# Optimization experiments

Measured on AMD Instinct MI355X. Metric: run time of the kernel, lower is better.

The kernel has to match this reference:

```python
import math
import jax, jax.numpy as jnp
import numpy as np

B, S, H, V = 8, 1024, 768, 8192  # V = max_verses

def setup_inputs() -> dict:
    key = jax.random.key(0)
    k1, k2, k3, k4 = jax.random.split(key, 4)
    hidden_states = jax.random.normal(k1, (B, S, H), dtype=jnp.float32)
    verse_ids = jax.random.randint(k2, (B, S), 0, V + 1)  # 0 = no verse
    cross_ref_matrix = jax.random.normal(k3, (V + 1, V + 1), dtype=jnp.float32) * 0.02
    out_w = jax.random.normal(k4, (H, H), dtype=jnp.float32) * (1.0 / math.sqrt(H))
    out_b = jnp.zeros((H,), dtype=jnp.float32)
    ln_w = jnp.ones((H,), dtype=jnp.float32)
    ln_b = jnp.zeros((H,), dtype=jnp.float32)
    return {"hidden_states": hidden_states, "verse_ids": verse_ids,
            "cross_ref_matrix": cross_ref_matrix, "out_w": out_w, "out_b": out_b,
            "ln_w": ln_w, "ln_b": ln_b}

def _layer_norm(x, w, b, eps=1e-5):
    mu = jnp.mean(x, axis=-1, keepdims=True)
    var = jnp.var(x, axis=-1, keepdims=True)
    return (x - mu) * jax.lax.rsqrt(var + eps) * w + b

def reference(hidden_states, verse_ids, cross_ref_matrix, out_w, out_b, ln_w, ln_b):
    h = hidden_states.shape[-1]
    has = verse_ids > 0                              # [B,S]
    # position_scores[b,i,j] = M[verse_ids[b,i], verse_ids[b,j]] where both have a verse, else 0
    scores = cross_ref_matrix[verse_ids[:, :, None], verse_ids[:, None, :]]  # [B,S,S] gather
    mask = has[:, :, None] & has[:, None, :]
    scores = jnp.where(mask, scores, 0.0) * (1.0 / math.sqrt(h))
    # NOTE: faithful to original — masked entries are 0 (NOT -inf) inside the softmax
    attn = jax.nn.softmax(scores, axis=-1)           # [B,S,S]; dropout is identity at eval
    ctx = jnp.einsum('bij,bjd->bid', attn, hidden_states)  # bmm
    proj = jnp.einsum('bid,od->bio', ctx, out_w) + out_b   # torch Linear: x @ W^T + b
    return _layer_norm(hidden_states + proj, ln_w, ln_b)
```

## Files before the change

### kernel.cpp

```cpp
#include <hip/hip_runtime.h>
#include <hip/hip_bf16.h>


namespace {
constexpr int kS = 1024;
constexpr int kH = 768;
constexpr int kV = 8193;
}

typedef __attribute__((ext_vector_type(8))) short short8;
typedef __attribute__((ext_vector_type(4))) float f32x4;

__device__ __forceinline__ unsigned short f2bf(float f) {
  union { float f; unsigned u; } v; v.f = f;
  unsigned r = v.u + 0x7FFFu + ((v.u >> 16) & 1u);
  return (unsigned short)(r >> 16);
}

__device__ __forceinline__ void async_lds16(const void* gsrc, void* ldst) {
  __builtin_amdgcn_global_load_lds(
      (const __attribute__((address_space(1))) unsigned int*)gsrc,
      (__attribute__((address_space(3))) unsigned int*)ldst, 16, 0, 0);
}

__global__ __launch_bounds__(256) void convert_w(const float* __restrict__ w,
                                                 unsigned short* __restrict__ wb) {
  int i = blockIdx.x * 256 + threadIdx.x;
  float4 v = reinterpret_cast<const float4*>(w)[i];
  ushort4 o;
  o.x = f2bf(v.x); o.y = f2bf(v.y); o.z = f2bf(v.z); o.w = f2bf(v.w);
  reinterpret_cast<ushort4*>(wb)[i] = o;
}

__global__ __launch_bounds__(256) void gather_softmax(const int* __restrict__ ids,
                                                      const float* __restrict__ Mx,
                                                      unsigned short* __restrict__ P) {
  const int i = blockIdx.x, b = blockIdx.y;
  const int t = threadIdx.x;
  const int sid = ids[b * kS + i];
  const float scale = 0.036084391824351615f;
  const float* Mrow = Mx + (long)sid * kV;
  float e[4];
  float lsum = 0.f;
#pragma unroll
  for (int q = 0; q < 4; ++q) {
    int j = t + q * 256;
    int cj = ids[b * kS + j];
    float v = 1.0f;
    if (sid > 0 && cj > 0) v = __expf(Mrow[cj] * scale);
    e[q] = v; lsum += v;
  }
#pragma unroll
  for (int o = 32; o; o >>= 1) lsum += __shfl_down(lsum, o);
  __shared__ float red[4];
  if ((t & 63) == 0) red[t >> 6] = lsum;
  __syncthreads();
  float denom = red[0] + red[1] + red[2] + red[3];
  float inv = 1.0f / denom;
  unsigned short* Pr = P + ((long)b * kS + i) * kS;
#pragma unroll
  for (int q = 0; q < 4; ++q) Pr[t + q * 256] = f2bf(e[q] * inv);
}

__global__ __launch_bounds__(256) void transpose_h(const float* __restrict__ hidden,
                                                   unsigned short* __restrict__ hT) {
  __shared__ float tile[32][33];
  const int b = blockIdx.z;
  const int h0 = blockIdx.x * 32;
  const int s0 = blockIdx.y * 32;
  const int t = threadIdx.x;
  const int c = t & 31, r0 = t >> 5;
  const float* src = hidden + (long)b * kS * kH;
#pragma unroll
  for (int q = 0; q < 4; ++q) {
    int r = r0 + q * 8;
    tile[r][c] = src[(long)(s0 + r) * kH + h0 + c];
  }
  __syncthreads();
  unsigned short* dst = hT + (long)b * kH * kS;
#pragma unroll
  for (int q = 0; q < 4; ++q) {
    int hh = r0 + q * 8;
    dst[(long)(h0 + hh) * kS + s0 + c] = f2bf(tile[c][hh]);
  }
}

__global__ __launch_bounds__(256) void gemm_nt(
    const unsigned short* __restrict__ A, long aBatchStride,
    const unsigned short* __restrict__ Bt, long bBatchStride,
    unsigned short* __restrict__ Cb, float* __restrict__ Cf,
    long cBatchStride, int N, int K, int outIsBf16) {
  __shared__ __align__(1024) unsigned short lds[6144];
  const int b = blockIdx.z;
  const int bn = blockIdx.x, bm = blockIdx.y;
  const unsigned short* Ab = A + (long)b * aBatchStride;
  const unsigned short* Bb = Bt + (long)b * bBatchStride;
  const int t = threadIdx.x;
  const int w = t >> 6, lane = t & 63;
  const int wr = w >> 1, wc = w & 1;
  const int lrow = lane & 15, kq = lane >> 4;

  const int r = t >> 2, ch = t & 3;
  const unsigned short* gA = Ab + (long)(bm * 64 + r) * K + ch * 8;
  const unsigned short* gB0 = Bb + (long)(bn * 128 + r) * K + ch * 8;
  const unsigned short* gB1 = gB0 + (long)64 * K;
  unsigned short* ldsA_dst = &lds[w * 512];
  unsigned short* ldsB0_dst = &lds[2048 + w * 512];
  unsigned short* ldsB1_dst = &lds[4096 + w * 512];

  f32x4 acc[2][4];
#pragma unroll
  for (int mi = 0; mi < 2; ++mi)
#pragma unroll
    for (int ni = 0; ni < 4; ++ni) acc[mi][ni] = (f32x4){0.f, 0.f, 0.f, 0.f};

  const int nk = K >> 5;
  for (int kt = 0; kt < nk; ++kt) {
    async_lds16(gA, ldsA_dst);
    async_lds16(gB0, ldsB0_dst);
    async_lds16(gB1, ldsB1_dst);
    gA += 32; gB0 += 32; gB1 += 32;
    __syncthreads();
    short8 af[2], bfr[4];
#pragma unroll
    for (int mi = 0; mi < 2; ++mi)
      af[mi] = *reinterpret_cast<const short8*>(&lds[(wr * 32 + mi * 16 + lrow) * 32 + kq * 8]);
#pragma unroll
    for (int ni = 0; ni < 4; ++ni)
      bfr[ni] = *reinterpret_cast<const short8*>(&lds[2048 + (wc * 64 + ni * 16 + lrow) * 32 + kq * 8]);
#pragma unroll
    for (int mi = 0; mi < 2; ++mi)
#pragma unroll
      for (int ni = 0; ni < 4; ++ni)
        acc[mi][ni] = __builtin_amdgcn_mfma_f32_16x16x32_bf16(af[mi], bfr[ni], acc[mi][ni], 0, 0, 0);
    __syncthreads();
  }

  const int row0 = bm * 64 + wr * 32;
  const int col0 = bn * 128 + wc * 64;
#pragma unroll
  for (int mi = 0; mi < 2; ++mi)
#pragma unroll
    for (int ni = 0; ni < 4; ++ni)
#pragma unroll
      for (int rg = 0; rg < 4; ++rg) {
        int row = row0 + mi * 16 + kq * 4 + rg;
        int col = col0 + ni * 16 + lrow;
        long off = (long)b * cBatchStride + (long)row * N + col;
        float v = acc[mi][ni][rg];
        if (outIsBf16) Cb[off] = f2bf(v);
        else Cf[off] = v;
      }
}

__global__ __launch_bounds__(256) void residual_ln(
    const float* __restrict__ hidden, const float* __restrict__ proj,
    const float* __restrict__ ob, const float* __restrict__ lw,
    const float* __restrict__ lb, float* __restrict__ out) {
  const long row = blockIdx.x;
  const float* h = hidden + row * kH;
  const float* p = proj + row * kH;
  const int t = threadIdx.x;
  float x[3];
  float s = 0.f, sq = 0.f;
#pragma unroll
  for (int q = 0; q < 3; ++q) {
    int c = t + q * 256;
    float v = h[c] + p[c] + ob[c];
    x[q] = v; s += v; sq += v * v;
  }
#pragma unroll
  for (int o = 32; o; o >>= 1) { s += __shfl_down(s, o); sq += __shfl_down(sq, o); }
  __shared__ float rs[4], rq[4];
  if ((t & 63) == 0) { rs[t >> 6] = s; rq[t >> 6] = sq; }
  __syncthreads();
  float ts = rs[0] + rs[1] + rs[2] + rs[3];
  float tq = rq[0] + rq[1] + rq[2] + rq[3];
  const float invH = 1.0f / 768.0f;
  float mu = ts * invH;
  float var = tq * invH - mu * mu;
  float rstd = rsqrtf(var + 1e-5f);
#pragma unroll
  for (int q = 0; q < 3; ++q) {
    int c = t + q * 256;
    out[row * kH + c] = (x[q] - mu) * rstd * lw[c] + lb[c];
  }
}

extern "C" void kernel_launch(void* const* d_in, const int* in_sizes, int n_in,
                              void* d_out, int out_size, void* d_ws, size_t ws_size,
                              hipStream_t stream) {
  const float* hidden = (const float*)d_in[0];
  const int* ids      = (const int*)d_in[1];
  const float* Mx     = (const float*)d_in[2];
  const float* out_w  = (const float*)d_in[3];
  const float* out_b  = (const float*)d_in[4];
  const float* ln_w   = (const float*)d_in[5];
  const float* ln_b   = (const float*)d_in[6];
  float* out = (float*)d_out;

  char* ws = (char*)d_ws;
  const long szP = 16777216L, szHT = 12582912L, szCTX = 12582912L;
  unsigned short* P   = (unsigned short*)ws;
  unsigned short* hT  = (unsigned short*)(ws + szP);
  unsigned short* ctx = (unsigned short*)(ws + szP + szHT);
  unsigned short* Wb  = (unsigned short*)(ws + szP + szHT + szCTX);
  float* proj = (float*)ws;

  convert_w<<<576, 256, 0, stream>>>(out_w, Wb);
  gather_softmax<<<dim3(1024, 8), 256, 0, stream>>>(ids, Mx, P);
  transpose_h<<<dim3(24, 32, 8), 256, 0, stream>>>(hidden, hT);
  gemm_nt<<<dim3(6, 16, 8), 256, 0, stream>>>(
      P, (long)kS * kS, hT, (long)kH * kS, ctx, nullptr, (long)kS * kH, kH, kS, 1);
  gemm_nt<<<dim3(6, 16, 8), 256, 0, stream>>>(
      ctx, (long)kS * kH, Wb, 0L, nullptr, proj, (long)kS * kH, kH, kH, 0);
  residual_ln<<<8192, 256, 0, stream>>>(hidden, proj, out_b, ln_w, ln_b, out);
}
```

Baseline: 469.2 us.

## Stage cross-ref row in LDS, enlarge GEMM tiles, vectorize softmax store and LayerNorm

The gather-softmax kernel now copies the whole 8193-float cross-reference row into LDS with coalesced loads, loads the verse ids as int4, and stores probabilities as ushort4. This replaces scattered global gathers. The GEMM block tile grows from 64x128 to 128x128, with a 4x4 MFMA fragment per wave and the output type made a template parameter. This raises data reuse per LDS load but halves the block count. The residual LayerNorm uses 192 threads with float4 loads and stores. Staging the row costs 32KB of LDS per block and copies the full row even though only 1024 entries are read, which may lower occupancy and add memory traffic.

```diff
diff --git a/kernel.cpp b/kernel.cpp
--- a/kernel.cpp
+++ b/kernel.cpp
@@ -35,31 +35,39 @@
 __global__ __launch_bounds__(256) void gather_softmax(const int* __restrict__ ids,
                                                       const float* __restrict__ Mx,
                                                       unsigned short* __restrict__ P) {
+  __shared__ float row[kV];
+  __shared__ float red[4];
   const int i = blockIdx.x, b = blockIdx.y;
   const int t = threadIdx.x;
   const int sid = ids[b * kS + i];
+  if (sid > 0) {
+    const float* src = Mx + (long)sid * kV;
+#pragma unroll
+    for (int q = 0; q < 32; ++q) row[t + q * 256] = src[t + q * 256];
+    if (t == 0) row[8192] = src[8192];
+  }
+  __syncthreads();
+  const int4 cj4 = reinterpret_cast<const int4*>(ids + b * kS)[t];
+  const int cj[4] = {cj4.x, cj4.y, cj4.z, cj4.w};
   const float scale = 0.036084391824351615f;
-  const float* Mrow = Mx + (long)sid * kV;
   float e[4];
   float lsum = 0.f;
 #pragma unroll
   for (int q = 0; q < 4; ++q) {
-    int j = t + q * 256;
-    int cj = ids[b * kS + j];
     float v = 1.0f;
-    if (sid > 0 && cj > 0) v = __expf(Mrow[cj] * scale);
+    if (sid > 0 && cj[q] > 0) v = __expf(row[cj[q]] * scale);
     e[q] = v; lsum += v;
   }
 #pragma unroll
   for (int o = 32; o; o >>= 1) lsum += __shfl_down(lsum, o);
-  __shared__ float red[4];
   if ((t & 63) == 0) red[t >> 6] = lsum;
   __syncthreads();
-  float denom = red[0] + red[1] + red[2] + red[3];
-  float inv = 1.0f / denom;
-  unsigned short* Pr = P + ((long)b * kS + i) * kS;
-#pragma unroll
-  for (int q = 0; q < 4; ++q) Pr[t + q * 256] = f2bf(e[q] * inv);
+  const float denom = red[0] + red[1] + red[2] + red[3];
+  const float inv = 1.0f / denom;
+  ushort4 o;
+  o.x = f2bf(e[0] * inv); o.y = f2bf(e[1] * inv);
+  o.z = f2bf(e[2] * inv); o.w = f2bf(e[3] * inv);
+  reinterpret_cast<ushort4*>(P + ((long)b * kS + i) * kS)[t] = o;
 }
 
 __global__ __launch_bounds__(256) void transpose_h(const float* __restrict__ hidden,
@@ -85,106 +93,100 @@
   }
 }
 
+template <int OUT_BF16>
 __global__ __launch_bounds__(256) void gemm_nt(
-    const unsigned short* __restrict__ A, long aBatchStride,
-    const unsigned short* __restrict__ Bt, long bBatchStride,
-    unsigned short* __restrict__ Cb, float* __restrict__ Cf,
-    long cBatchStride, int N, int K, int outIsBf16) {
-  __shared__ __align__(1024) unsigned short lds[6144];
-  const int b = blockIdx.z;
-  const int bn = blockIdx.x, bm = blockIdx.y;
-  const unsigned short* Ab = A + (long)b * aBatchStride;
-  const unsigned short* Bb = Bt + (long)b * bBatchStride;
-  const int t = threadIdx.x;
-  const int w = t >> 6, lane = t & 63;
-  const int wr = w >> 1, wc = w & 1;
+    const unsigned short* __restrict__ A, long aStride,
+    const unsigned short* __restrict__ Bt, long bStride,
+    void* __restrict__ C, long cStride, int N, int K) {
+  __shared__ __align__(1024) unsigned short lds[8192];
+  const int b = blockIdx.z, bn = blockIdx.x, bm = blockIdx.y;
+  const unsigned short* Ab = A + (long)b * aStride + (long)(bm * 128) * K;
+  const unsigned short* Bb = Bt + (long)b * bStride + (long)(bn * 128) * K;
+  const int t = threadIdx.x;
+  const int lane = t & 63;
+  const int wr = (t >> 7) & 1, wc = (t >> 6) & 1;
   const int lrow = lane & 15, kq = lane >> 4;
-
-  const int r = t >> 2, ch = t & 3;
-  const unsigned short* gA = Ab + (long)(bm * 64 + r) * K + ch * 8;
-  const unsigned short* gB0 = Bb + (long)(bn * 128 + r) * K + ch * 8;
-  const unsigned short* gB1 = gB0 + (long)64 * K;
-  unsigned short* ldsA_dst = &lds[w * 512];
-  unsigned short* ldsB0_dst = &lds[2048 + w * 512];
-  unsigned short* ldsB1_dst = &lds[4096 + w * 512];
-
-  f32x4 acc[2][4];
-#pragma unroll
-  for (int mi = 0; mi < 2; ++mi)
+  const int srow = t >> 2, scol = (t & 3) * 8;
+  char* ldsb = (char*)lds;
+
+  f32x4 acc[4][4];
+#pragma unroll
+  for (int mi = 0; mi < 4; ++mi)
 #pragma unroll
     for (int ni = 0; ni < 4; ++ni) acc[mi][ni] = (f32x4){0.f, 0.f, 0.f, 0.f};
 
-  const int nk = K >> 5;
-  for (int kt = 0; kt < nk; ++kt) {
-    async_lds16(gA, ldsA_dst);
-    async_lds16(gB0, ldsB0_dst);
-    async_lds16(gB1, ldsB1_dst);
-    gA += 32; gB0 += 32; gB1 += 32;
+  for (int kt = 0; kt < K; kt += 32) {
+#pragma unroll
+    for (int q = 0; q < 2; ++q) {
+      async_lds16(Ab + (long)(srow + q * 64) * K + kt + scol, ldsb + t * 16 + q * 4096);
+      async_lds16(Bb + (long)(srow + q * 64) * K + kt + scol, ldsb + 8192 + t * 16 + q * 4096);
+    }
     __syncthreads();
-    short8 af[2], bfr[4];
-#pragma unroll
-    for (int mi = 0; mi < 2; ++mi)
-      af[mi] = *reinterpret_cast<const short8*>(&lds[(wr * 32 + mi * 16 + lrow) * 32 + kq * 8]);
+    short8 af[4], bf[4];
+#pragma unroll
+    for (int mi = 0; mi < 4; ++mi)
+      af[mi] = *reinterpret_cast<const short8*>(&lds[(wr * 64 + mi * 16 + lrow) * 32 + kq * 8]);
 #pragma unroll
     for (int ni = 0; ni < 4; ++ni)
-      bfr[ni] = *reinterpret_cast<const short8*>(&lds[2048 + (wc * 64 + ni * 16 + lrow) * 32 + kq * 8]);
-#pragma unroll
-    for (int mi = 0; mi < 2; ++mi)
+      bf[ni] = *reinterpret_cast<const short8*>(&lds[4096 + (wc * 64 + ni * 16 + lrow) * 32 + kq * 8]);
+#pragma unroll
+    for (int mi = 0; mi < 4; ++mi)
 #pragma unroll
       for (int ni = 0; ni < 4; ++ni)
-        acc[mi][ni] = __builtin_amdgcn_mfma_f32_16x16x32_bf16(af[mi], bfr[ni], acc[mi][ni], 0, 0, 0);
+        acc[mi][ni] = __builtin_amdgcn_mfma_f32_16x16x32_bf16(af[mi], bf[ni], acc[mi][ni], 0, 0, 0);
     __syncthreads();
   }
 
-  const int row0 = bm * 64 + wr * 32;
+  const int row0 = bm * 128 + wr * 64;
   const int col0 = bn * 128 + wc * 64;
 #pragma unroll
-  for (int mi = 0; mi < 2; ++mi)
+  for (int mi = 0; mi < 4; ++mi)
 #pragma unroll
     for (int ni = 0; ni < 4; ++ni)
 #pragma unroll
       for (int rg = 0; rg < 4; ++rg) {
-        int row = row0 + mi * 16 + kq * 4 + rg;
-        int col = col0 + ni * 16 + lrow;
-        long off = (long)b * cBatchStride + (long)row * N + col;
+        int r = row0 + mi * 16 + kq * 4 + rg;
+        int c = col0 + ni * 16 + lrow;
+        long off = (long)b * cStride + (long)r * N + c;
         float v = acc[mi][ni][rg];
-        if (outIsBf16) Cb[off] = f2bf(v);
-        else Cf[off] = v;
+        if (OUT_BF16) ((unsigned short*)C)[off] = f2bf(v);
+        else ((float*)C)[off] = v;
       }
 }
 
-__global__ __launch_bounds__(256) void residual_ln(
+__global__ __launch_bounds__(192) void residual_ln(
     const float* __restrict__ hidden, const float* __restrict__ proj,
     const float* __restrict__ ob, const float* __restrict__ lw,
     const float* __restrict__ lb, float* __restrict__ out) {
   const long row = blockIdx.x;
-  const float* h = hidden + row * kH;
-  const float* p = proj + row * kH;
-  const int t = threadIdx.x;
-  float x[3];
-  float s = 0.f, sq = 0.f;
-#pragma unroll
-  for (int q = 0; q < 3; ++q) {
-    int c = t + q * 256;
-    float v = h[c] + p[c] + ob[c];
-    x[q] = v; s += v; sq += v * v;
-  }
+  const int t = threadIdx.x;
+  float4 hv = reinterpret_cast<const float4*>(hidden + row * kH)[t];
+  float4 pv = reinterpret_cast<const float4*>(proj + row * kH)[t];
+  float4 bv = reinterpret_cast<const float4*>(ob)[t];
+  float4 x;
+  x.x = hv.x + pv.x + bv.x; x.y = hv.y + pv.y + bv.y;
+  x.z = hv.z + pv.z + bv.z; x.w = hv.w + pv.w + bv.w;
+  float s = x.x + x.y + x.z + x.w;
+  float sq = x.x * x.x + x.y * x.y + x.z * x.z + x.w * x.w;
 #pragma unroll
   for (int o = 32; o; o >>= 1) { s += __shfl_down(s, o); sq += __shfl_down(sq, o); }
-  __shared__ float rs[4], rq[4];
+  __shared__ float rs[3], rq[3];
   if ((t & 63) == 0) { rs[t >> 6] = s; rq[t >> 6] = sq; }
   __syncthreads();
-  float ts = rs[0] + rs[1] + rs[2] + rs[3];
-  float tq = rq[0] + rq[1] + rq[2] + rq[3];
+  const float ts = rs[0] + rs[1] + rs[2];
+  const float tq = rq[0] + rq[1] + rq[2];
   const float invH = 1.0f / 768.0f;
-  float mu = ts * invH;
-  float var = tq * invH - mu * mu;
-  float rstd = rsqrtf(var + 1e-5f);
-#pragma unroll
-  for (int q = 0; q < 3; ++q) {
-    int c = t + q * 256;
-    out[row * kH + c] = (x[q] - mu) * rstd * lw[c] + lb[c];
-  }
+  const float mu = ts * invH;
+  const float var = tq * invH - mu * mu;
+  const float rstd = rsqrtf(var + 1e-5f);
+  float4 wv = reinterpret_cast<const float4*>(lw)[t];
+  float4 lv = reinterpret_cast<const float4*>(lb)[t];
+  float4 o4;
+  o4.x = (x.x - mu) * rstd * wv.x + lv.x;
+  o4.y = (x.y - mu) * rstd * wv.y + lv.y;
+  o4.z = (x.z - mu) * rstd * wv.z + lv.z;
+  o4.w = (x.w - mu) * rstd * wv.w + lv.w;
+  reinterpret_cast<float4*>(out + row * kH)[t] = o4;
 }
 
 extern "C" void kernel_launch(void* const* d_in, const int* in_sizes, int n_in,
@@ -210,9 +212,9 @@
   convert_w<<<576, 256, 0, stream>>>(out_w, Wb);
   gather_softmax<<<dim3(1024, 8), 256, 0, stream>>>(ids, Mx, P);
   transpose_h<<<dim3(24, 32, 8), 256, 0, stream>>>(hidden, hT);
-  gemm_nt<<<dim3(6, 16, 8), 256, 0, stream>>>(
-      P, (long)kS * kS, hT, (long)kH * kS, ctx, nullptr, (long)kS * kH, kH, kS, 1);
-  gemm_nt<<<dim3(6, 16, 8), 256, 0, stream>>>(
-      ctx, (long)kS * kH, Wb, 0L, nullptr, proj, (long)kS * kH, kH, kH, 0);
-  residual_ln<<<8192, 256, 0, stream>>>(hidden, proj, out_b, ln_w, ln_b, out);
-}
+  gemm_nt<1><<<dim3(6, 8, 8), 256, 0, stream>>>(
+      P, (long)kS * kS, hT, (long)kH * kS, ctx, (long)kS * kH, kH, kS);
+  gemm_nt<0><<<dim3(6, 8, 8), 256, 0, stream>>>(
+      ctx, (long)kS * kH, Wb, 0L, proj, (long)kS * kH, kH, kH);
+  residual_ln<<<8192, 192, 0, stream>>>(hidden, proj, out_b, ln_w, ln_b, out);
+}
```

Measured after the change: 444.6 us. 1.06x faster.
